# Kernel optimization log

Hardware: AMD Instinct MI355X
Metric: run time of the kernel (lower is better)

Reference implementation:

```python
import jax, jax.numpy as jnp
import numpy as np

ALPHA = 0.1
MARGIN = 1.0
SLOPE = 0.2  # LeakyReLU negative_slope
OFFSET = 1.0e6

def leaky(x):
    return jnp.where(x >= 0, x, SLOPE * x)

def _xavier(key, shape, gain=np.sqrt(2.0)):
    fan_out, fan_in = shape[0], shape[1]
    std = gain * np.sqrt(2.0 / (fan_in + fan_out))
    return jax.random.normal(key, shape, dtype=jnp.float32) * std

def setup_inputs() -> dict:
    key = jax.random.key(0)
    ks = jax.random.split(key, 8)
    B, F, T, D, H = 32768, 128, 32, 16, 10
    return {
        "X": jax.random.normal(ks[0], (B, F), dtype=jnp.float32),
        "affine_weights": jax.random.normal(ks[1], (T, F, D), dtype=jnp.float32),
        "W0": _xavier(ks[2], (H, D)),
        "W1": _xavier(ks[3], (H, H)),
        "W2": _xavier(ks[4], (H, H)),
        "W3": _xavier(ks[5], (H, H)),
        "Wh": _xavier(ks[6], (T, H)),
        "bh": jnp.zeros((T,), dtype=jnp.float32),
    }

def reference(X, affine_weights, W0, W1, W2, W3, Wh, bh):
    T = affine_weights.shape[0]
    # goad_transforms: x_trans [B, trans_dim, n_trans]; labels[b,t] = t (implicit)
    x_trans = jnp.einsum('bn,ant->bta', X, affine_weights)
    # ConvNet encoder, kernel_size=1 convs == per-position channel matmuls
    h = jnp.einsum('od,bdt->bot', W0, x_trans)
    for W in (W1, W2, W3):
        h = jnp.einsum('od,bdt->bot', W, leaky(h))
    rep = h                                   # [B, H, T]
    # head: LeakyReLU + Conv1d(H->T, bias=True)
    pred = jnp.einsum('oh,bht->bot', Wh, leaky(rep)) + bh[None, :, None]  # [B, T, T]
    batch_rep = jnp.transpose(rep, (0, 2, 1))  # [B, T, H]
    # CrossEntropy(reduction='none') with labels[b,t]=t -> -diag of log_softmax over class dim
    logp = jax.nn.log_softmax(pred, axis=1)
    loss_ce = -jnp.diagonal(logp, axis1=1, axis2=2)          # [B, T]
    # triplet center loss
    means = jnp.mean(batch_rep, axis=0)                       # [T, H]
    res = jnp.sum((batch_rep[:, :, None, :] - means[None, None, :, :]) ** 2, axis=-1)  # [B,T,T]
    pos = jnp.diagonal(res, axis1=1, axis2=2)                 # [B, T]
    neg = jnp.min(res + jnp.eye(T, dtype=res.dtype) * OFFSET, axis=-1)  # [B, T]
    loss_tc = jnp.mean(jnp.maximum(pos + MARGIN - neg, 0.0))  # scalar
    loss = jnp.mean(ALPHA * loss_tc + loss_ce, axis=1)        # [B]
    return batch_rep, loss
```

## Files before the change

### kernel.cpp

```cpp
#include <hip/hip_runtime.h>

typedef __attribute__((ext_vector_type(8))) short bf16x8;
typedef __attribute__((ext_vector_type(4))) float f32x4;

#define BTOT 32768
#define FDIM 128
#define TDIM 32
#define DDIM 16
#define HDIM 10
#define CDIM 320
#define ALPHA_C 0.1f
#define MARGIN_C 1.0f
#define SLOPE_C 0.2f
#define OFFSET_C 1.0e6f

#define WS_A0BF 0
#define WS_MEAN 20480
#define WS_TC   20800
#define WS_CE   20864

#define R1SZ 21504
#define LDS_TOTAL (R1SZ + 21760)

__device__ __forceinline__ float leaky(float x) { return x >= 0.f ? x : SLOPE_C * x; }

__device__ __forceinline__ unsigned short f2bf(float f) {
    unsigned int u = __float_as_uint(f);
    u += 0x7fffu + ((u >> 16) & 1u);
    return (unsigned short)(u >> 16);
}

__global__ void prep_kernel(const float* __restrict__ aw, const float* __restrict__ W0,
                            unsigned short* __restrict__ a0bf) {
    int idx = blockIdx.x * blockDim.x + threadIdx.x;
    if (idx >= CDIM * FDIM) return;
    int c = idx >> 7, n = idx & 127;
    int t = c / HDIM, o = c - t * HDIM;
    const float* a = aw + ((size_t)t * FDIM + n) * DDIM;
    const float* w = W0 + o * DDIM;
    float s = 0.f;
#pragma unroll
    for (int d = 0; d < DDIM; ++d) s += a[d] * w[d];
    a0bf[idx] = f2bf(s);
}

__global__ __launch_bounds__(256) void gemm0_fused(
    const float* __restrict__ X, const unsigned short* __restrict__ a0bf,
    const float* __restrict__ W1, const float* __restrict__ W2,
    const float* __restrict__ W3, const float* __restrict__ Wh,
    const float* __restrict__ bh,
    float* __restrict__ rep, float* __restrict__ ce_acc,
    float* __restrict__ mean_acc)
{
    __shared__ __align__(16) char ldsbuf[LDS_TOTAL];
    unsigned short (*xs)[136]  = (unsigned short (*)[136])ldsbuf;
    float          (*ys)[84]   = (float (*)[84])ldsbuf;
    unsigned short (*a0s)[136] = (unsigned short (*)[136])(ldsbuf + R1SZ);
    float          (*mpart)[80]= (float (*)[80])(ldsbuf + R1SZ);

    int tid = threadIdx.x;
    int bchunk = blockIdx.x >> 2, cchunk = blockIdx.x & 3;
    int b0 = bchunk * 64, c0 = cchunk * 80;

#pragma unroll
    for (int k = 0; k < 8; ++k) {
        int idx = tid + k * 256;
        int row = idx >> 5, col4 = idx & 31;
        float4 v = reinterpret_cast<const float4*>(X + (size_t)(b0 + row) * FDIM)[col4];
        uint2 pk;
        pk.x = (unsigned)f2bf(v.x) | ((unsigned)f2bf(v.y) << 16);
        pk.y = (unsigned)f2bf(v.z) | ((unsigned)f2bf(v.w) << 16);
        *reinterpret_cast<uint2*>(&xs[row][col4 * 4]) = pk;
    }
#pragma unroll
    for (int k = 0; k < 5; ++k) {
        int idx = tid + k * 256;
        int row = idx >> 4, j = idx & 15;
        uint4 v = reinterpret_cast<const uint4*>(a0bf + (size_t)(c0 + row) * FDIM)[j];
        *reinterpret_cast<uint4*>(&a0s[row][j * 8]) = v;
    }
    __syncthreads();

    int lane = tid & 63, w = tid >> 6;
    int r16 = lane & 15, g = lane >> 4;
    bf16x8 af[4];
#pragma unroll
    for (int s = 0; s < 4; ++s)
        af[s] = *reinterpret_cast<const bf16x8*>(&xs[w * 16 + r16][s * 32 + g * 8]);
    __syncthreads();

#pragma unroll
    for (int ct = 0; ct < 5; ++ct) {
        f32x4 acc = {0.f, 0.f, 0.f, 0.f};
#pragma unroll
        for (int s = 0; s < 4; ++s) {
            bf16x8 bfrag = *reinterpret_cast<const bf16x8*>(&a0s[ct * 16 + r16][s * 32 + g * 8]);
            acc = __builtin_amdgcn_mfma_f32_16x16x32_bf16(af[s], bfrag, acc, 0, 0, 0);
        }
#pragma unroll
        for (int r = 0; r < 4; ++r)
            ys[w * 16 + g * 4 + r][ct * 16 + r16] = acc[r];
    }
    __syncthreads();

    int t8 = tid & 7;
    int t  = cchunk * 8 + t8;
    float mgg[HDIM];
#pragma unroll
    for (int o = 0; o < HDIM; ++o) mgg[o] = 0.f;

#pragma unroll
    for (int p = 0; p < 2; ++p) {
        int bl = (tid >> 3) + p * 32;
        float* yrow = &ys[bl][t8 * HDIM];
        float h[HDIM], lh[HDIM], gg[HDIM];
#pragma unroll
        for (int q = 0; q < 5; ++q) {
            float2 v = reinterpret_cast<const float2*>(yrow)[q];
            h[2 * q] = v.x; h[2 * q + 1] = v.y;
        }
#pragma unroll
        for (int o = 0; o < HDIM; ++o) lh[o] = leaky(h[o]);
#pragma unroll
        for (int o = 0; o < HDIM; ++o) { float s = 0.f;
#pragma unroll
            for (int i = 0; i < HDIM; ++i) s += W1[o * HDIM + i] * lh[i]; gg[o] = s; }
#pragma unroll
        for (int o = 0; o < HDIM; ++o) lh[o] = leaky(gg[o]);
#pragma unroll
        for (int o = 0; o < HDIM; ++o) { float s = 0.f;
#pragma unroll
            for (int i = 0; i < HDIM; ++i) s += W2[o * HDIM + i] * lh[i]; h[o] = s; }
#pragma unroll
        for (int o = 0; o < HDIM; ++o) lh[o] = leaky(h[o]);
#pragma unroll
        for (int o = 0; o < HDIM; ++o) { float s = 0.f;
#pragma unroll
            for (int i = 0; i < HDIM; ++i) s += W3[o * HDIM + i] * lh[i]; gg[o] = s; }

#pragma unroll
        for (int q = 0; q < 5; ++q) {
            float2 v; v.x = gg[2 * q]; v.y = gg[2 * q + 1];
            reinterpret_cast<float2*>(yrow)[q] = v;
        }
#pragma unroll
        for (int o = 0; o < HDIM; ++o) mgg[o] += gg[o];

#pragma unroll
        for (int o = 0; o < HDIM; ++o) lh[o] = leaky(gg[o]);
        float m = -1e30f, se = 0.f, pt = 0.f;
#pragma unroll
        for (int o = 0; o < TDIM; ++o) {
            float s = bh[o];
#pragma unroll
            for (int i = 0; i < HDIM; ++i) s += Wh[o * HDIM + i] * lh[i];
            pt = (o == t) ? s : pt;
            float nm = fmaxf(m, s);
            se = se * __expf(m - nm) + __expf(s - nm);
            m = nm;
        }
        float ce = m + __logf(se) - pt;
        ce += __shfl_xor(ce, 1, 64);
        ce += __shfl_xor(ce, 2, 64);
        ce += __shfl_xor(ce, 4, 64);
        if (t8 == 0) atomicAdd(&ce_acc[b0 + bl], ce);
    }

#pragma unroll
    for (int o = 0; o < HDIM; ++o) mpart[tid >> 3][t8 * HDIM + o] = mgg[o];
    __syncthreads();

#pragma unroll
    for (int k = 0; k < 5; ++k) {
        int idx = tid + k * 256;
        int row = idx / 20, j = idx - row * 20;
        float4 v = *reinterpret_cast<const float4*>(&ys[row][j * 4]);
        reinterpret_cast<float4*>(rep + (size_t)(b0 + row) * CDIM + c0)[j] = v;
    }
    if (tid < 80) {
        float s = 0.f;
#pragma unroll
        for (int r = 0; r < 32; ++r) s += mpart[r][tid];
        atomicAdd(&mean_acc[c0 + tid], s);
    }
}

__global__ __launch_bounds__(256) void tc_kernel(const float* __restrict__ rep,
    const float* __restrict__ mean_acc, float* __restrict__ tc_sum)
{
    __shared__ float tile[32][CDIM];
    __shared__ float mm[CDIM];
    __shared__ float msq[TDIM];
    __shared__ float wpart[4];
    int tid = threadIdx.x;
    int b0 = blockIdx.x * 32;

    for (int i = tid; i < CDIM; i += 256) mm[i] = mean_acc[i] * (1.f / BTOT);
    const float4* src = reinterpret_cast<const float4*>(rep + (size_t)b0 * CDIM);
#pragma unroll
    for (int k = 0; k < 10; ++k) {
        int idx = tid + k * 256;
        int row = idx / 80, col4 = idx - row * 80;
        *reinterpret_cast<float4*>(&tile[row][col4 * 4]) = src[idx];
    }
    __syncthreads();
    if (tid < TDIM) {
        float s = 0.f;
#pragma unroll
        for (int h = 0; h < HDIM; ++h) { float v = mm[tid * HDIM + h]; s += v * v; }
        msq[tid] = s;
    }
    __syncthreads();

    int t = tid & 31, bg = tid >> 5;
    float rv[4][HDIM], rsq[4];
#pragma unroll
    for (int j = 0; j < 4; ++j) {
        const float* rp = &tile[bg * 4 + j][t * HDIM];
        float s = 0.f;
#pragma unroll
        for (int q = 0; q < 5; ++q) {
            float2 v = reinterpret_cast<const float2*>(rp)[q];
            rv[j][2 * q] = v.x; rv[j][2 * q + 1] = v.y;
            s += v.x * v.x + v.y * v.y;
        }
        rsq[j] = s;
    }
    float pos[4], neg[4];
#pragma unroll
    for (int j = 0; j < 4; ++j) { pos[j] = 0.f; neg[j] = 1e30f; }
#pragma unroll 4
    for (int c = 0; c < TDIM; ++c) {
        float m0[HDIM];
#pragma unroll
        for (int q = 0; q < 5; ++q) {
            float2 v = reinterpret_cast<const float2*>(&mm[c * HDIM])[q];
            m0[2 * q] = v.x; m0[2 * q + 1] = v.y;
        }
        float mq = msq[c];
        bool isT = (c == t);
#pragma unroll
        for (int j = 0; j < 4; ++j) {
            float dot = 0.f;
#pragma unroll
            for (int h = 0; h < HDIM; ++h) dot += rv[j][h] * m0[h];
            float s = rsq[j] - 2.f * dot + mq;
            if (isT) pos[j] = s;
            float s2 = isT ? s + OFFSET_C : s;
            neg[j] = fminf(neg[j], s2);
        }
    }
    float hs = 0.f;
#pragma unroll
    for (int j = 0; j < 4; ++j) hs += fmaxf(pos[j] + MARGIN_C - neg[j], 0.f);
#pragma unroll
    for (int m = 1; m < 64; m <<= 1) hs += __shfl_xor(hs, m, 64);
    int lane = tid & 63, w = tid >> 6;
    if (lane == 0) wpart[w] = hs;
    __syncthreads();
    if (tid == 0) atomicAdd(tc_sum, wpart[0] + wpart[1] + wpart[2] + wpart[3]);
}

__global__ void final_kernel(const float* __restrict__ ce_acc,
                             const float* __restrict__ tc_sum, float* __restrict__ loss)
{
    int b = blockIdx.x * blockDim.x + threadIdx.x;
    if (b < BTOT)
        loss[b] = ALPHA_C * (tc_sum[0] * (1.f / ((float)BTOT * TDIM)))
                + ce_acc[b] * (1.f / TDIM);
}

extern "C" void kernel_launch(void* const* d_in, const int* in_sizes, int n_in,
                              void* d_out, int out_size, void* d_ws, size_t ws_size,
                              hipStream_t stream) {
    const float* X  = (const float*)d_in[0];
    const float* aw = (const float*)d_in[1];
    const float* W0 = (const float*)d_in[2];
    const float* W1 = (const float*)d_in[3];
    const float* W2 = (const float*)d_in[4];
    const float* W3 = (const float*)d_in[5];
    const float* Wh = (const float*)d_in[6];
    const float* bh = (const float*)d_in[7];
    float* ws = (float*)d_ws;
    unsigned short* a0bf = (unsigned short*)(ws + WS_A0BF);
    float* mean_acc = ws + WS_MEAN;
    float* tc_sum   = ws + WS_TC;
    float* ce_acc   = ws + WS_CE;
    float* out_rep = (float*)d_out;
    float* loss = out_rep + (size_t)BTOT * TDIM * HDIM;

    hipMemsetAsync(mean_acc, 0, (384 + BTOT) * sizeof(float), stream);
    prep_kernel<<<(CDIM * FDIM) / 256, 256, 0, stream>>>(aw, W0, a0bf);
    gemm0_fused<<<2048, 256, 0, stream>>>(X, a0bf, W1, W2, W3, Wh, bh,
                                          out_rep, ce_acc, mean_acc);
    tc_kernel<<<BTOT / 32, 256, 0, stream>>>(out_rep, mean_acc, tc_sum);
    final_kernel<<<BTOT / 256, 256, 0, stream>>>(ce_acc, tc_sum, loss);
}
```

Baseline: 89.35 us.

## Pad LDS layouts, write rep directly, cheaper online softmax and bf16 pack

The fused GEMM kernel pads its LDS staging rows (one extra float per 10-element group, and an odd stride for the mean partials) to reduce bank conflicts. Each thread now writes its rep values straight to global memory instead of staging them back through LDS and copying them out afterward. The online softmax uses a single exp per step instead of two, X is packed to bf16 with the hardware v_cvt_pk_bf16_f32 instruction, and leaky uses fmaxf. A launch-bounds occupancy hint is added. The direct rep stores are float2 with a stride of 40 bytes per thread, which may coalesce worse than the previous float4 copy.

```diff
diff --git a/kernel.cpp b/kernel.cpp
--- a/kernel.cpp
+++ b/kernel.cpp
@@ -19,10 +19,12 @@
 #define WS_TC   20800
 #define WS_CE   20864
 
-#define R1SZ 21504
-#define LDS_TOTAL (R1SZ + 21760)
-
-__device__ __forceinline__ float leaky(float x) { return x >= 0.f ? x : SLOPE_C * x; }
+#define R2OFF 23552
+#define LDS_TOTAL (R2OFF + 21760)
+#define YSROW 92
+#define MPROW 81
+
+__device__ __forceinline__ float leaky(float x) { return fmaxf(x, SLOPE_C * x); }
 
 __device__ __forceinline__ unsigned short f2bf(float f) {
     unsigned int u = __float_as_uint(f);
@@ -44,7 +46,7 @@
     a0bf[idx] = f2bf(s);
 }
 
-__global__ __launch_bounds__(256) void gemm0_fused(
+__global__ __launch_bounds__(256, 3) void gemm0_fused(
     const float* __restrict__ X, const unsigned short* __restrict__ a0bf,
     const float* __restrict__ W1, const float* __restrict__ W2,
     const float* __restrict__ W3, const float* __restrict__ Wh,
@@ -54,9 +56,9 @@
 {
     __shared__ __align__(16) char ldsbuf[LDS_TOTAL];
     unsigned short (*xs)[136]  = (unsigned short (*)[136])ldsbuf;
-    float          (*ys)[84]   = (float (*)[84])ldsbuf;
-    unsigned short (*a0s)[136] = (unsigned short (*)[136])(ldsbuf + R1SZ);
-    float          (*mpart)[80]= (float (*)[80])(ldsbuf + R1SZ);
+    float* ysf = (float*)ldsbuf;
+    unsigned short (*a0s)[136] = (unsigned short (*)[136])(ldsbuf + R2OFF);
+    float* mpartf = (float*)(ldsbuf + R2OFF);
 
     int tid = threadIdx.x;
     int bchunk = blockIdx.x >> 2, cchunk = blockIdx.x & 3;
@@ -67,9 +69,10 @@
         int idx = tid + k * 256;
         int row = idx >> 5, col4 = idx & 31;
         float4 v = reinterpret_cast<const float4*>(X + (size_t)(b0 + row) * FDIM)[col4];
-        uint2 pk;
-        pk.x = (unsigned)f2bf(v.x) | ((unsigned)f2bf(v.y) << 16);
-        pk.y = (unsigned)f2bf(v.z) | ((unsigned)f2bf(v.w) << 16);
+        unsigned pk0, pk1;
+        asm("v_cvt_pk_bf16_f32 %0, %1, %2" : "=v"(pk0) : "v"(v.x), "v"(v.y));
+        asm("v_cvt_pk_bf16_f32 %0, %1, %2" : "=v"(pk1) : "v"(v.z), "v"(v.w));
+        uint2 pk; pk.x = pk0; pk.y = pk1;
         *reinterpret_cast<uint2*>(&xs[row][col4 * 4]) = pk;
     }
 #pragma unroll
@@ -81,7 +84,7 @@
     }
     __syncthreads();
 
-    int lane = tid & 63, w = tid >> 6;
+    int lane = tid & 63, w = __builtin_amdgcn_readfirstlane(tid >> 6);
     int r16 = lane & 15, g = lane >> 4;
     bf16x8 af[4];
 #pragma unroll
@@ -97,28 +100,27 @@
             bf16x8 bfrag = *reinterpret_cast<const bf16x8*>(&a0s[ct * 16 + r16][s * 32 + g * 8]);
             acc = __builtin_amdgcn_mfma_f32_16x16x32_bf16(af[s], bfrag, acc, 0, 0, 0);
         }
-#pragma unroll
-        for (int r = 0; r < 4; ++r)
-            ys[w * 16 + g * 4 + r][ct * 16 + r16] = acc[r];
-    }
-    __syncthreads();
-
-    int t8 = tid & 7;
-    int t  = cchunk * 8 + t8;
+        int c = ct * 16 + r16;
+        int cpad = c + c / 10;
+        int ybase = (w * 16 + g * 4) * YSROW + cpad;
+#pragma unroll
+        for (int r = 0; r < 4; ++r) ysf[ybase + r * YSROW] = acc[r];
+    }
+    __syncthreads();
+
+    int t8 = tid & 7, bl0 = tid >> 3;
+    int t = cchunk * 8 + t8;
     float mgg[HDIM];
 #pragma unroll
     for (int o = 0; o < HDIM; ++o) mgg[o] = 0.f;
 
 #pragma unroll
     for (int p = 0; p < 2; ++p) {
-        int bl = (tid >> 3) + p * 32;
-        float* yrow = &ys[bl][t8 * HDIM];
+        int bl = bl0 + p * 32;
+        const float* yrow = ysf + bl * YSROW + t8 * 11;
         float h[HDIM], lh[HDIM], gg[HDIM];
 #pragma unroll
-        for (int q = 0; q < 5; ++q) {
-            float2 v = reinterpret_cast<const float2*>(yrow)[q];
-            h[2 * q] = v.x; h[2 * q + 1] = v.y;
-        }
+        for (int q = 0; q < HDIM; ++q) h[q] = yrow[q];
 #pragma unroll
         for (int o = 0; o < HDIM; ++o) lh[o] = leaky(h[o]);
 #pragma unroll
@@ -138,10 +140,11 @@
 #pragma unroll
             for (int i = 0; i < HDIM; ++i) s += W3[o * HDIM + i] * lh[i]; gg[o] = s; }
 
+        float* rp = rep + (size_t)(b0 + bl) * CDIM + c0 + t8 * 10;
 #pragma unroll
         for (int q = 0; q < 5; ++q) {
             float2 v; v.x = gg[2 * q]; v.y = gg[2 * q + 1];
-            reinterpret_cast<float2*>(yrow)[q] = v;
+            reinterpret_cast<float2*>(rp)[q] = v;
         }
 #pragma unroll
         for (int o = 0; o < HDIM; ++o) mgg[o] += gg[o];
@@ -155,9 +158,12 @@
 #pragma unroll
             for (int i = 0; i < HDIM; ++i) s += Wh[o * HDIM + i] * lh[i];
             pt = (o == t) ? s : pt;
-            float nm = fmaxf(m, s);
-            se = se * __expf(m - nm) + __expf(s - nm);
-            m = nm;
+            float d = s - m;
+            float e = __expf(-fabsf(d));
+            float ra = d > 0.f ? e : 1.f;
+            float rb = d > 0.f ? 1.f : e;
+            se = se * ra + rb;
+            m = fmaxf(m, s);
         }
         float ce = m + __logf(se) - pt;
         ce += __shfl_xor(ce, 1, 64);
@@ -167,20 +173,12 @@
     }
 
 #pragma unroll
-    for (int o = 0; o < HDIM; ++o) mpart[tid >> 3][t8 * HDIM + o] = mgg[o];
-    __syncthreads();
-
-#pragma unroll
-    for (int k = 0; k < 5; ++k) {
-        int idx = tid + k * 256;
-        int row = idx / 20, j = idx - row * 20;
-        float4 v = *reinterpret_cast<const float4*>(&ys[row][j * 4]);
-        reinterpret_cast<float4*>(rep + (size_t)(b0 + row) * CDIM + c0)[j] = v;
-    }
+    for (int o = 0; o < HDIM; ++o) mpartf[bl0 * MPROW + t8 * HDIM + o] = mgg[o];
+    __syncthreads();
     if (tid < 80) {
         float s = 0.f;
 #pragma unroll
-        for (int r = 0; r < 32; ++r) s += mpart[r][tid];
+        for (int r = 0; r < 32; ++r) s += mpartf[r * MPROW + tid];
         atomicAdd(&mean_acc[c0 + tid], s);
     }
 }
```

Result: no change. 90.83 us (+1.7%).
